# Performance work log

Measured on AMD Instinct MI355X. Metric: run time of the kernel, lower is better.

The kernel has to match this reference:

```python
import jax, jax.numpy as jnp
import numpy as np

N_HEADS = 32
N_KV_HEADS = 8
HEAD_DIM = 128
ROPE_THETA = 10000.0


def _rope(x, position_ids):
    # x: [B, n_heads, T, hd], position_ids: [B, T]
    hd = x.shape[-1]
    inv_freq = 1.0 / (ROPE_THETA ** (jnp.arange(0, hd, 2, dtype=jnp.float32) / hd))  # [hd/2]
    ang = position_ids.astype(jnp.float32)[:, :, None] * inv_freq[None, None, :]  # [B, T, hd/2]
    emb = jnp.concatenate([ang, ang], axis=-1)  # [B, T, hd] (HF layout)
    cos = jnp.cos(emb)[:, None, :, :]
    sin = jnp.sin(emb)[:, None, :, :]
    x1, x2 = x[..., : hd // 2], x[..., hd // 2 :]
    rot = jnp.concatenate([-x2, x1], axis=-1)
    return x * cos + rot * sin


def setup_inputs() -> dict:
    key = jax.random.key(0)
    ks = jax.random.split(key, 9)
    B, T, D = 16, 1, 4096
    PAST = 4095
    S = PAST + T
    w = 0.02
    return {
        "hidden_states": jax.random.normal(ks[0], (B, T, D), jnp.float32),
        "attention_mask": jnp.zeros((B, 1, T, S), jnp.float32),  # additive mask, all visible
        "position_ids": jnp.full((B, T), PAST, dtype=jnp.int64),
        "past_key": jax.random.normal(ks[1], (B, N_KV_HEADS, PAST, HEAD_DIM), jnp.float32),
        "past_value": jax.random.normal(ks[2], (B, N_KV_HEADS, PAST, HEAD_DIM), jnp.float32),
        "Wq": jax.random.normal(ks[3], (N_HEADS * HEAD_DIM, D), jnp.float32) * w,
        "Wk": jax.random.normal(ks[4], (N_KV_HEADS * HEAD_DIM, D), jnp.float32) * w,
        "Wv": jax.random.normal(ks[5], (N_KV_HEADS * HEAD_DIM, D), jnp.float32) * w,
        "Wo": jax.random.normal(ks[6], (D, N_HEADS * HEAD_DIM), jnp.float32) * w,
    }


def reference(hidden_states, attention_mask, position_ids, past_key, past_value, Wq, Wk, Wv, Wo):
    B, T, D = hidden_states.shape
    hd = HEAD_DIM
    # q/k/v projections (Llama: no bias)
    q = jnp.einsum("btd,ed->bte", hidden_states, Wq).reshape(B, T, N_HEADS, hd).transpose(0, 2, 1, 3)
    k_new = jnp.einsum("btd,ed->bte", hidden_states, Wk).reshape(B, T, N_KV_HEADS, hd).transpose(0, 2, 1, 3)
    v_new = jnp.einsum("btd,ed->bte", hidden_states, Wv).reshape(B, T, N_KV_HEADS, hd).transpose(0, 2, 1, 3)
    # RoPE on the new token(s); past cache entries are already rotated
    q = _rope(q, position_ids)
    k_new = _rope(k_new, position_ids)
    # static-cache update: write new K/V at position past_seq_len (append)
    k_cache = jnp.concatenate([past_key, k_new], axis=2)   # [B, n_kv, S, hd]
    v_cache = jnp.concatenate([past_value, v_new], axis=2)
    # GQA: repeat kv heads
    n_rep = N_HEADS // N_KV_HEADS
    k = jnp.repeat(k_cache, n_rep, axis=1)  # [B, H, S, hd]
    v = jnp.repeat(v_cache, n_rep, axis=1)
    scores = jnp.einsum("bhtd,bhsd->bhts", q, k) / jnp.sqrt(jnp.float32(hd))
    scores = scores + attention_mask  # additive mask [B,1,T,S]
    w_attn = jax.nn.softmax(scores, axis=-1)
    ctx = jnp.einsum("bhts,bhsd->bhtd", w_attn, v)  # [B, H, T, hd]
    ctx = ctx.transpose(0, 2, 1, 3).reshape(B, T, N_HEADS * hd)
    attn_output = jnp.einsum("bte,de->btd", ctx, Wo)
    return attn_output, k_cache, v_cache
```

## Files before the change

### kernel.cpp

```cpp
#include <hip/hip_runtime.h>

#define NB 16
#define DMODEL 4096
#define NH 32
#define NKV 8
#define HD 128
#define SEQ 4096
#define PASTN 4095
#define EQKV 6144
#define NCHUNK 16
#define CHUNKS 256
#define PSTRIDE 136
#define SCALE 0.08838834764831845f

typedef float v4f __attribute__((ext_vector_type(4)));

__global__ __launch_bounds__(256) void qkv_proj(
    const float* __restrict__ hs, const float* __restrict__ Wq,
    const float* __restrict__ Wk, const float* __restrict__ Wv,
    float* __restrict__ raw ) {
  __shared__ __align__(16) float ld[2][16][256];
  __shared__ __align__(16) float red[4][32][33];
  const int tid = threadIdx.x, wid = tid >> 6, lane = tid & 63;
  const int e0 = blockIdx.x * 8 + wid * 2;
  const int fo = lane * 4;

  const float* wrow[2];
#pragma unroll
  for (int r = 0; r < 2; ++r) {
    int e = e0 + r;
    wrow[r] = (e < 4096) ? (Wq + (size_t)e * DMODEL)
            : (e < 5120) ? (Wk + (size_t)(e - 4096) * DMODEL)
                         : (Wv + (size_t)(e - 5120) * DMODEL);
  }

  float acc[2][16];
#pragma unroll
  for (int r = 0; r < 2; ++r)
#pragma unroll
    for (int b = 0; b < 16; ++b) acc[r][b] = 0.f;

  v4f st[4];
#pragma unroll
  for (int i = 0; i < 4; ++i)
    st[i] = *(const v4f*)(hs + (size_t)(i * 4 + wid) * DMODEL + fo);
#pragma unroll
  for (int i = 0; i < 4; ++i)
    *(v4f*)(&ld[0][i * 4 + wid][fo]) = st[i];
  v4f w4[2];
#pragma unroll
  for (int r = 0; r < 2; ++r) w4[r] = *(const v4f*)(wrow[r] + fo);
  __syncthreads();

  for (int c = 0; c < 16; ++c) {
    const int k1 = (c + 1) * 256;
    v4f w4n[2];
    if (c < 15) {
#pragma unroll
      for (int i = 0; i < 4; ++i)
        st[i] = *(const v4f*)(hs + (size_t)(i * 4 + wid) * DMODEL + k1 + fo);
#pragma unroll
      for (int r = 0; r < 2; ++r) w4n[r] = *(const v4f*)(wrow[r] + k1 + fo);
    }
    const float* lb = &ld[c & 1][0][0];
#pragma unroll
    for (int b = 0; b < 16; ++b) {
      v4f h4 = *(const v4f*)(lb + b * 256 + fo);
#pragma unroll
      for (int r = 0; r < 2; ++r) {
        v4f t = w4[r] * h4;
        acc[r][b] += t[0] + t[1] + t[2] + t[3];
      }
    }
    if (c < 15) {
#pragma unroll
      for (int i = 0; i < 4; ++i)
        *(v4f*)(&ld[(c + 1) & 1][i * 4 + wid][fo]) = st[i];
      w4[0] = w4n[0];
      w4[1] = w4n[1];
    }
    __syncthreads();
  }

#pragma unroll
  for (int r = 0; r < 2; ++r)
#pragma unroll
    for (int b = 0; b < 16; ++b) acc[r][b] += __shfl_xor(acc[r][b], 32);

  if (lane < 32) {
#pragma unroll
    for (int r = 0; r < 2; ++r)
#pragma unroll
      for (int b = 0; b < 16; ++b)
        red[wid][lane][r * 16 + b] = acc[r][b];
  }
  __syncthreads();
  if (lane < 32) {
    float s = 0.f;
#pragma unroll
    for (int t2 = 0; t2 < 32; ++t2) s += red[wid][t2][lane];
    const int r = lane >> 4, bb = lane & 15;
    raw[(size_t)bb * EQKV + e0 + r] = s;
  }
}

__device__ __forceinline__ float rope_val(const float* src, int d, float pos) {
  int i = d & 63;
  float inv_freq = powf(10000.f, -(float)(2 * i) * (1.f / 128.f));
  float ang = pos * inv_freq;
  float s, c;
  sincosf(ang, &s, &c);
  float x = src[d];
  float rot = (d < 64) ? -src[d + 64] : src[d - 64];
  return x * c + rot * s;
}

__global__ void rope_scatter(const float* __restrict__ raw,
                             const void* __restrict__ pos_ids,
                             float* __restrict__ qout,
                             float* __restrict__ kc, float* __restrict__ vc) {
  const int b = blockIdx.y, j = blockIdx.x, d = threadIdx.x;
  const int* pi = (const int*)pos_ids;
  long long pos = (pi[1] == 0 && pi[0] != 0) ? ((const long long*)pos_ids)[b]
                                             : (long long)pi[b];
  const float fpos = (float)pos;
  if (j < 32) {
    const float* src = raw + (size_t)b * EQKV + j * HD;
    qout[(size_t)b * (NH * HD) + j * HD + d] = rope_val(src, d, fpos);
  } else if (j < 40) {
    int kvh = j - 32;
    const float* src = raw + (size_t)b * EQKV + 4096 + kvh * HD;
    kc[(((size_t)b * NKV + kvh) * SEQ + PASTN) * HD + d] = rope_val(src, d, fpos);
  } else {
    int kvh = j - 40;
    vc[(((size_t)b * NKV + kvh) * SEQ + PASTN) * HD + d] =
        raw[(size_t)b * EQKV + 5120 + kvh * HD + d];
  }
}

__global__ __launch_bounds__(256, 4) void attn_decode(
    const float* __restrict__ pastK, const float* __restrict__ pastV,
    const float* __restrict__ qv, const float* __restrict__ mask,
    float* __restrict__ kc, float* __restrict__ vc,
    float* __restrict__ part ) {
  __shared__ __align__(16) float sm[4][4][132];

  const int chunk = blockIdx.x, kv = blockIdx.y, b = blockIdx.z;
  const int tid = threadIdx.x, wid = tid >> 6, lane = tid & 63;
  const int half = lane >> 5, q32 = lane & 31;
  const int fo = q32 * 4;

  v4f q[4];
  const float* qb = qv + (size_t)b * (NH * HD) + kv * 4 * HD + fo;
#pragma unroll
  for (int h = 0; h < 4; ++h) q[h] = *(const v4f*)(qb + h * HD);

  const size_t prow = ((size_t)b * NKV + kv) * PASTN;
  const size_t crow = ((size_t)b * NKV + kv) * SEQ;
  const int base = chunk * CHUNKS + wid * (CHUNKS / 4);
  const float* mrow = mask + (size_t)b * SEQ;

  const float mreg = mrow[base + 2 * q32 + half];

  float m[4], l[4];
  v4f c[4];
#pragma unroll
  for (int h = 0; h < 4; ++h) {
    m[h] = -1e30f; l[h] = 0.f;
    c[h] = (v4f){0.f, 0.f, 0.f, 0.f};
  }

  v4f kq[4], vq[4];
#pragma unroll
  for (int i = 0; i < 4; ++i) {
    const int s = base + 2 * i + half;
    const float* kp = (s < PASTN) ? pastK + (prow + s) * HD + fo
                                  : kc + (crow + s) * HD + fo;
    const float* vp = (s < PASTN) ? pastV + (prow + s) * HD + fo
                                  : vc + (crow + s) * HD + fo;
    kq[i] = __builtin_nontemporal_load((const v4f*)kp);
    vq[i] = __builtin_nontemporal_load((const v4f*)vp);
  }

#pragma unroll 4
  for (int t = 0; t < 32; ++t) {
    const int sp = base + 2 * t;
    const int s = sp + half;
    const v4f kch = kq[t & 3], vch = vq[t & 3];
    if (t < 28) {
      const int s2 = sp + 8 + half;
      const float* kp = (s2 < PASTN) ? pastK + (prow + s2) * HD + fo
                                     : kc + (crow + s2) * HD + fo;
      const float* vp = (s2 < PASTN) ? pastV + (prow + s2) * HD + fo
                                     : vc + (crow + s2) * HD + fo;
      kq[t & 3] = __builtin_nontemporal_load((const v4f*)kp);
      vq[t & 3] = __builtin_nontemporal_load((const v4f*)vp);
    }
    if (s < PASTN) {
      __builtin_nontemporal_store(kch, (v4f*)(kc + (crow + s) * HD + fo));
      __builtin_nontemporal_store(vch, (v4f*)(vc + (crow + s) * HD + fo));
    }

    const float mval = __shfl(mreg, t | (lane & 32));

    float d4[4];
#pragma unroll
    for (int h = 0; h < 4; ++h) {
      v4f tv = q[h] * kch;
      d4[h] = tv[0] + tv[1] + tv[2] + tv[3];
    }
#pragma unroll
    for (int off = 1; off <= 16; off <<= 1)
#pragma unroll
      for (int h = 0; h < 4; ++h) d4[h] += __shfl_xor(d4[h], off);

#pragma unroll
    for (int h = 0; h < 4; ++h) {
      float sc = d4[h] * SCALE + mval;
      if (sc > m[h]) {
        float alpha = __expf(m[h] - sc);
        l[h] *= alpha;
        c[h] *= alpha;
        m[h] = sc;
      }
      float p = __expf(sc - m[h]);
      l[h] += p;
      c[h] += p * vch;
    }
  }

#pragma unroll
  for (int h = 0; h < 4; ++h) {
    float mo = __shfl_xor(m[h], 32);
    float mn = fmaxf(m[h], mo);
    float f = __expf(m[h] - mn);
    l[h] *= f;
    c[h] *= f;
    l[h] += __shfl_xor(l[h], 32);
#pragma unroll
    for (int j = 0; j < 4; ++j) c[h][j] += __shfl_xor(c[h][j], 32);
    m[h] = mn;
  }

  if (half == 0) {
#pragma unroll
    for (int h = 0; h < 4; ++h) {
      if (q32 == 0) { sm[wid][h][0] = m[h]; sm[wid][h][1] = l[h]; }
      *(v4f*)(&sm[wid][h][4 + fo]) = c[h];
    }
  }
  __syncthreads();

  float mstar = -1e30f;
#pragma unroll
  for (int sl = 0; sl < 4; ++sl) mstar = fmaxf(mstar, sm[sl][wid][0]);
  float den = 0.f;
  const int d2 = lane * 2;
  float nx = 0.f, ny = 0.f;
#pragma unroll
  for (int sl = 0; sl < 4; ++sl) {
    float w = __expf(sm[sl][wid][0] - mstar);
    den += w * sm[sl][wid][1];
    nx += w * sm[sl][wid][4 + d2];
    ny += w * sm[sl][wid][4 + d2 + 1];
  }
  float* pp = part + (((size_t)b * NH + kv * 4 + wid) * NCHUNK + chunk) * PSTRIDE;
  if (lane == 0) { pp[0] = mstar; pp[1] = den; }
  float2 nv = {nx, ny};
  *(float2*)(pp + 4 + d2) = nv;
}

__global__ void combine(const float* __restrict__ part, float* __restrict__ ctx) {
  const int bh = blockIdx.x;
  const int lane = threadIdx.x;
  const float* pp = part + (size_t)bh * NCHUNK * PSTRIDE;
  float mstar = -1e30f;
#pragma unroll
  for (int c = 0; c < NCHUNK; ++c) mstar = fmaxf(mstar, pp[c * PSTRIDE]);
  float den = 0.f, nx = 0.f, ny = 0.f;
  const int d2 = lane * 2;
#pragma unroll
  for (int c = 0; c < NCHUNK; ++c) {
    float w = __expf(pp[c * PSTRIDE] - mstar);
    den += w * pp[c * PSTRIDE + 1];
    float2 pv = *(const float2*)(pp + c * PSTRIDE + 4 + d2);
    nx += w * pv.x;
    ny += w * pv.y;
  }
  float inv = 1.0f / den;
  ctx[(size_t)bh * HD + d2] = nx * inv;
  ctx[(size_t)bh * HD + d2 + 1] = ny * inv;
}

__global__ __launch_bounds__(256) void out_proj(
    const float* __restrict__ ctx, const float* __restrict__ Wo,
    float* __restrict__ out) {
  __shared__ __align__(16) float ld[2][16][256];
  __shared__ __align__(16) float red[4][32][33];
  const int tid = threadIdx.x, wid = tid >> 6, lane = tid & 63;
  const int e0 = blockIdx.x * 8 + wid * 2;
  const int fo = lane * 4;

  float acc[2][16];
#pragma unroll
  for (int r = 0; r < 2; ++r)
#pragma unroll
    for (int b = 0; b < 16; ++b) acc[r][b] = 0.f;

  v4f st[4];
#pragma unroll
  for (int i = 0; i < 4; ++i)
    st[i] = *(const v4f*)(ctx + (size_t)(i * 4 + wid) * DMODEL + fo);
#pragma unroll
  for (int i = 0; i < 4; ++i)
    *(v4f*)(&ld[0][i * 4 + wid][fo]) = st[i];
  v4f w4[2];
#pragma unroll
  for (int r = 0; r < 2; ++r)
    w4[r] = *(const v4f*)(Wo + (size_t)(e0 + r) * DMODEL + fo);
  __syncthreads();

  for (int c = 0; c < 16; ++c) {
    const int k1 = (c + 1) * 256;
    v4f w4n[2];
    if (c < 15) {
#pragma unroll
      for (int i = 0; i < 4; ++i)
        st[i] = *(const v4f*)(ctx + (size_t)(i * 4 + wid) * DMODEL + k1 + fo);
#pragma unroll
      for (int r = 0; r < 2; ++r)
        w4n[r] = *(const v4f*)(Wo + (size_t)(e0 + r) * DMODEL + k1 + fo);
    }
    const float* lb = &ld[c & 1][0][0];
#pragma unroll
    for (int b = 0; b < 16; ++b) {
      v4f h4 = *(const v4f*)(lb + b * 256 + fo);
#pragma unroll
      for (int r = 0; r < 2; ++r) {
        v4f t = w4[r] * h4;
        acc[r][b] += t[0] + t[1] + t[2] + t[3];
      }
    }
    if (c < 15) {
#pragma unroll
      for (int i = 0; i < 4; ++i)
        *(v4f*)(&ld[(c + 1) & 1][i * 4 + wid][fo]) = st[i];
      w4[0] = w4n[0];
      w4[1] = w4n[1];
    }
    __syncthreads();
  }

#pragma unroll
  for (int r = 0; r < 2; ++r)
#pragma unroll
    for (int b = 0; b < 16; ++b) acc[r][b] += __shfl_xor(acc[r][b], 32);

  if (lane < 32) {
#pragma unroll
    for (int r = 0; r < 2; ++r)
#pragma unroll
      for (int b = 0; b < 16; ++b)
        red[wid][lane][r * 16 + b] = acc[r][b];
  }
  __syncthreads();
  if (lane < 32) {
    float s = 0.f;
#pragma unroll
    for (int t2 = 0; t2 < 32; ++t2) s += red[wid][t2][lane];
    const int r = lane >> 4, bb = lane & 15;
    out[(size_t)bb * DMODEL + e0 + r] = s;
  }
}

extern "C" void kernel_launch(void* const* d_in, const int* in_sizes, int n_in,
                              void* d_out, int out_size, void* d_ws, size_t ws_size,
                              hipStream_t stream) {
  const float* hs    = (const float*)d_in[0];
  const float* mask  = (const float*)d_in[1];
  const void*  pos   = d_in[2];
  const float* pastK = (const float*)d_in[3];
  const float* pastV = (const float*)d_in[4];
  const float* Wq    = (const float*)d_in[5];
  const float* Wk    = (const float*)d_in[6];
  const float* Wv    = (const float*)d_in[7];
  const float* Wo    = (const float*)d_in[8];

  float* out  = (float*)d_out;
  float* attn = out;
  float* kc   = out + (size_t)NB * DMODEL;
  float* vc   = kc + (size_t)NB * NKV * SEQ * HD;

  float* ws      = (float*)d_ws;
  float* ws_q    = ws;
  float* ws_raw  = ws_q + (size_t)NB * NH * HD;
  float* ws_part = ws_raw + (size_t)NB * EQKV;
  float* ws_ctx  = ws_part + (size_t)NB * NH * NCHUNK * PSTRIDE;

  qkv_proj<<<EQKV / 8, 256, 0, stream>>>(hs, Wq, Wk, Wv, ws_raw);
  rope_scatter<<<dim3(48, NB), 128, 0, stream>>>(ws_raw, pos, ws_q, kc, vc);
  attn_decode<<<dim3(NCHUNK, NKV, NB), 256, 0, stream>>>(pastK, pastV, ws_q, mask,
                                                         kc, vc, ws_part);
  combine<<<NB * NH, 64, 0, stream>>>(ws_part, ws_ctx);
  out_proj<<<DMODEL / 8, 256, 0, stream>>>(ws_ctx, Wo, attn);
}
```

Measured before the change: 268.0 us.

## Split attention into a QK score pass and an exact-max PV pass

The single online-softmax loop becomes two passes. The first streams K, computes scores and keeps one score per lane. A wave-wide max reduction then gives the exact maximum, and the second pass streams V with a fixed max. This removes the per-step rescaling branches and the cross-half max merge. In exchange, K and V loads are serialized rather than interleaved, which lowers memory-level parallelism per wave in a bandwidth-bound kernel.

```diff
diff --git a/kernel.cpp b/kernel.cpp
--- a/kernel.cpp
+++ b/kernel.cpp
@@ -162,84 +162,104 @@
 
   const float mreg = mrow[base + 2 * q32 + half];
 
+  float keep[4];
+
+  {
+    v4f kq[4];
+#pragma unroll
+    for (int i = 0; i < 4; ++i) {
+      const int s = base + 2 * i + half;
+      const float* kp = (s < PASTN) ? pastK + (prow + s) * HD + fo
+                                    : kc + (crow + s) * HD + fo;
+      kq[i] = __builtin_nontemporal_load((const v4f*)kp);
+    }
+
+#pragma unroll 4
+    for (int t = 0; t < 32; ++t) {
+      const int sp = base + 2 * t;
+      const int s = sp + half;
+      const v4f kch = kq[t & 3];
+      if (t < 28) {
+        const int s2 = sp + 8 + half;
+        const float* kp = (s2 < PASTN) ? pastK + (prow + s2) * HD + fo
+                                       : kc + (crow + s2) * HD + fo;
+        kq[t & 3] = __builtin_nontemporal_load((const v4f*)kp);
+      }
+      if (s < PASTN)
+        __builtin_nontemporal_store(kch, (v4f*)(kc + (crow + s) * HD + fo));
+
+      const float mval = __shfl(mreg, t | (lane & 32));
+
+      float d4[4];
+#pragma unroll
+      for (int h = 0; h < 4; ++h) {
+        v4f tv = q[h] * kch;
+        d4[h] = tv[0] + tv[1] + tv[2] + tv[3];
+      }
+#pragma unroll
+      for (int off = 1; off <= 16; off <<= 1)
+#pragma unroll
+        for (int h = 0; h < 4; ++h) d4[h] += __shfl_xor(d4[h], off);
+
+#pragma unroll
+      for (int h = 0; h < 4; ++h) {
+        float sc = d4[h] * SCALE + mval;
+        if (q32 == t) keep[h] = sc;
+      }
+    }
+  }
+
   float m[4], l[4];
   v4f c[4];
 #pragma unroll
   for (int h = 0; h < 4; ++h) {
-    m[h] = -1e30f; l[h] = 0.f;
+    float mm = keep[h];
+#pragma unroll
+    for (int off = 1; off <= 32; off <<= 1)
+      mm = fmaxf(mm, __shfl_xor(mm, off));
+    m[h] = mm;
+    l[h] = 0.f;
     c[h] = (v4f){0.f, 0.f, 0.f, 0.f};
   }
 
-  v4f kq[4], vq[4];
-#pragma unroll
-  for (int i = 0; i < 4; ++i) {
-    const int s = base + 2 * i + half;
-    const float* kp = (s < PASTN) ? pastK + (prow + s) * HD + fo
-                                  : kc + (crow + s) * HD + fo;
-    const float* vp = (s < PASTN) ? pastV + (prow + s) * HD + fo
-                                  : vc + (crow + s) * HD + fo;
-    kq[i] = __builtin_nontemporal_load((const v4f*)kp);
-    vq[i] = __builtin_nontemporal_load((const v4f*)vp);
-  }
+  {
+    v4f vq[4];
+#pragma unroll
+    for (int i = 0; i < 4; ++i) {
+      const int s = base + 2 * i + half;
+      const float* vp = (s < PASTN) ? pastV + (prow + s) * HD + fo
+                                    : vc + (crow + s) * HD + fo;
+      vq[i] = __builtin_nontemporal_load((const v4f*)vp);
+    }
 
 #pragma unroll 4
-  for (int t = 0; t < 32; ++t) {
-    const int sp = base + 2 * t;
-    const int s = sp + half;
-    const v4f kch = kq[t & 3], vch = vq[t & 3];
-    if (t < 28) {
-      const int s2 = sp + 8 + half;
-      const float* kp = (s2 < PASTN) ? pastK + (prow + s2) * HD + fo
-                                     : kc + (crow + s2) * HD + fo;
-      const float* vp = (s2 < PASTN) ? pastV + (prow + s2) * HD + fo
-                                     : vc + (crow + s2) * HD + fo;
-      kq[t & 3] = __builtin_nontemporal_load((const v4f*)kp);
-      vq[t & 3] = __builtin_nontemporal_load((const v4f*)vp);
-    }
-    if (s < PASTN) {
-      __builtin_nontemporal_store(kch, (v4f*)(kc + (crow + s) * HD + fo));
-      __builtin_nontemporal_store(vch, (v4f*)(vc + (crow + s) * HD + fo));
-    }
-
-    const float mval = __shfl(mreg, t | (lane & 32));
-
-    float d4[4];
-#pragma unroll
-    for (int h = 0; h < 4; ++h) {
-      v4f tv = q[h] * kch;
-      d4[h] = tv[0] + tv[1] + tv[2] + tv[3];
-    }
-#pragma unroll
-    for (int off = 1; off <= 16; off <<= 1)
-#pragma unroll
-      for (int h = 0; h < 4; ++h) d4[h] += __shfl_xor(d4[h], off);
-
-#pragma unroll
-    for (int h = 0; h < 4; ++h) {
-      float sc = d4[h] * SCALE + mval;
-      if (sc > m[h]) {
-        float alpha = __expf(m[h] - sc);
-        l[h] *= alpha;
-        c[h] *= alpha;
-        m[h] = sc;
-      }
-      float p = __expf(sc - m[h]);
-      l[h] += p;
-      c[h] += p * vch;
+    for (int t = 0; t < 32; ++t) {
+      const int sp = base + 2 * t;
+      const int s = sp + half;
+      const v4f vch = vq[t & 3];
+      if (t < 28) {
+        const int s2 = sp + 8 + half;
+        const float* vp = (s2 < PASTN) ? pastV + (prow + s2) * HD + fo
+                                       : vc + (crow + s2) * HD + fo;
+        vq[t & 3] = __builtin_nontemporal_load((const v4f*)vp);
+      }
+      if (s < PASTN)
+        __builtin_nontemporal_store(vch, (v4f*)(vc + (crow + s) * HD + fo));
+
+#pragma unroll
+      for (int h = 0; h < 4; ++h) {
+        float p = __expf(__shfl(keep[h], t | (lane & 32)) - m[h]);
+        l[h] += p;
+        c[h] += p * vch;
+      }
     }
   }
 
 #pragma unroll
   for (int h = 0; h < 4; ++h) {
-    float mo = __shfl_xor(m[h], 32);
-    float mn = fmaxf(m[h], mo);
-    float f = __expf(m[h] - mn);
-    l[h] *= f;
-    c[h] *= f;
     l[h] += __shfl_xor(l[h], 32);
 #pragma unroll
     for (int j = 0; j < 4; ++j) c[h][j] += __shfl_xor(c[h][j], 32);
-    m[h] = mn;
   }
 
   if (half == 0) {
```

Result: faster. 254.3 us, median of 2 (-5.1%).
